# Kernel optimization log

Measured on AMD Instinct MI355X. Metric: run time of the kernel, lower is better.

The kernel has to match this reference:

```python
import jax, jax.numpy as jnp
import numpy as np

HEAD_DIM = 32
KERNEL = 9
DILATION = 3


def setup_inputs() -> dict:
    key = jax.random.key(0)
    k1, k2, k3 = jax.random.split(key, 3)
    B, d, L = 4, 512, 4096
    q = jax.random.normal(k1, (B, d, 1, L), dtype=jnp.float32)
    k = jax.random.normal(k2, (B, d, 1, L), dtype=jnp.float32)
    v = jax.random.normal(k3, (B, d, 1, L), dtype=jnp.float32)
    return {"q": q, "k": k, "v": v}


def reference(q, k, v):
    # q,k,v: [B, d, 1, L]; output: [B, 1, L, d]
    B, d, _, N = q.shape
    hd = HEAD_DIM
    h = d // hd
    K = KERNEL
    dil = DILATION
    pad = dil * (K - 1) // 2
    scale = hd ** -0.5

    # Window gather indices replicating nn.Unfold with zero padding.
    idx = jnp.arange(N)[:, None] + jnp.arange(K)[None, :] * dil - pad  # [N, K]
    valid = ((idx >= 0) & (idx < N)).astype(q.dtype)                   # [N, K]
    idxc = jnp.clip(idx, 0, N - 1)

    qr = q.reshape(B, h, hd, N)
    kr = k.reshape(B, h, hd, N)
    vr = v.reshape(B, h, hd, N)

    # Unfolded windows: [B, h, hd, N, K], zero outside bounds (like Unfold padding)
    kw = kr[:, :, :, idxc] * valid
    vw = vr[:, :, :, idxc] * valid

    attn = jnp.einsum('bhdn,bhdnk->bhnk', qr, kw) * scale
    attn = jax.nn.softmax(attn, axis=-1)
    out = jnp.einsum('bhnk,bhdnk->bhnd', attn, vw)  # [B, h, N, hd]
    # torch: transpose(1,2).reshape(B,1,N,d) -> heads concatenated per token
    return out.transpose(0, 2, 1, 3).reshape(B, 1, N, d)
```

## Files before the change

kernel.cpp:

```cpp
#include <hip/hip_runtime.h>
#include <math.h>

#define NPOS 4096
#define DCH  512
#define HD   32
#define NH   16
#define KW   9
#define DIL  3
#define PAD  12
#define TILE   32
#define NTILES (NPOS / TILE)
#define SPANT  (TILE + 2*PAD)
#define RS     60
#define ROWC   (RS / 4)
#define NCHK   (2 * HD * ROWC)
#define NINST  (NCHK / 64)
#define CSPL   8
#define CPT    (HD / CSPL)
#define TPT    4
#define WSPAN  28
#define NXCD   8

typedef float floatx4 __attribute__((ext_vector_type(4)));

__device__ __forceinline__ void gload16(const float* g, float* l) {
    __builtin_amdgcn_global_load_lds(
        (const __attribute__((address_space(1))) void*)g,
        (__attribute__((address_space(3))) void*)l,
        16, 0, 0);
}

__device__ __forceinline__ float dpp_sum8(float x) {
    int t;
    t = __builtin_amdgcn_update_dpp(0, __float_as_int(x), 0xB1, 0xF, 0xF, true);
    x += __int_as_float(t);
    t = __builtin_amdgcn_update_dpp(0, __float_as_int(x), 0x4E, 0xF, 0xF, true);
    x += __int_as_float(t);
    t = __builtin_amdgcn_update_dpp(0, __float_as_int(x), 0x141, 0xF, 0xF, true);
    x += __int_as_float(t);
    return x;
}

__device__ __forceinline__ void load_w(const float* base, float* w) {
    const float4* wp = (const float4*)base;
#pragma unroll
    for (int u = 0; u < WSPAN / 4; ++u) {
        float4 x = wp[u];
        w[4*u] = x.x; w[4*u+1] = x.y; w[4*u+2] = x.z; w[4*u+3] = x.w;
    }
}

__global__ __launch_bounds__(64) void dilate_attn_kernel(
    const float* __restrict__ q,
    const float* __restrict__ k,
    const float* __restrict__ v,
    float* __restrict__ out)
{
    __shared__ float kv[2 * HD * RS];

    const int id   = blockIdx.x;
    const int xcd  = id & (NXCD - 1);
    const int seq  = id >> 3;
    const int tile = seq & (NTILES - 1);
    const int bh   = ((seq >> 7) << 3) | xcd;

    const int n0t  = tile * TILE;
    const int ws   = n0t - PAD;

    const size_t cb = (size_t)bh * HD * NPOS;
    const float* qg = q + cb;
    const float* kg = k + cb;
    const float* vg = v + cb;

    const int tid = threadIdx.x;
    const int cs  = tid & (CSPL - 1);
    const int lg  = tid >> 3;
    const int n0  = n0t + lg * TPT;

    const float scale = 0.17677669529663687f;

    float4 qv[CPT];
#pragma unroll
    for (int i = 0; i < CPT; ++i)
        qv[i] = *(const float4*)(qg + (size_t)(cs * CPT + i) * NPOS + n0);
    asm volatile("" ::: "memory");

#pragma unroll
    for (int it = 0; it < NINST; ++it) {
        int c   = it * 64 + tid;
        int row = c / ROWC;
        int c4  = c - row * ROWC;
        int g0  = min(max(ws + c4 * 4, 0), NPOS - 4);
        const float* src = (row < HD)
            ? kg + (size_t)row * NPOS + g0
            : vg + (size_t)(row - HD) * NPOS + g0;
        gload16(src, &kv[c * 4]);
    }

    asm volatile("s_waitcnt vmcnt(7)" ::: "memory");

    float s[TPT][KW];
#pragma unroll
    for (int t = 0; t < TPT; ++t)
#pragma unroll
        for (int j = 0; j < KW; ++j) s[t][j] = 0.0f;

#pragma unroll
    for (int i = 0; i < CPT; ++i) {
        int row = cs * CPT + i;
        float w[WSPAN];
        load_w(&kv[row * RS + lg * TPT], w);
        float qt[TPT] = {qv[i].x, qv[i].y, qv[i].z, qv[i].w};
#pragma unroll
        for (int t = 0; t < TPT; ++t)
#pragma unroll
            for (int j = 0; j < KW; ++j)
                s[t][j] = fmaf(qt[t], w[t + 3*j], s[t][j]);
    }

#pragma unroll
    for (int t = 0; t < TPT; ++t)
#pragma unroll
        for (int j = 0; j < KW; ++j)
            s[t][j] = dpp_sum8(s[t][j]);

    const bool masked = (tile == 0) || (tile == NTILES - 1);
    if (!masked) {
#pragma unroll
        for (int t = 0; t < TPT; ++t) {
            float m = -INFINITY;
#pragma unroll
            for (int j = 0; j < KW; ++j) {
                float x = s[t][j] * scale;
                s[t][j] = x;
                m = fmaxf(m, x);
            }
            float sum = 0.0f;
#pragma unroll
            for (int j = 0; j < KW; ++j) {
                float e = __expf(s[t][j] - m);
                s[t][j] = e;
                sum += e;
            }
            float inv = 1.0f / sum;
#pragma unroll
            for (int j = 0; j < KW; ++j) s[t][j] *= inv;
        }
    } else {
#pragma unroll
        for (int t = 0; t < TPT; ++t) {
            float vm[KW];
            float m = -INFINITY;
#pragma unroll
            for (int j = 0; j < KW; ++j) {
                vm[j] = ((unsigned)(n0 + t + 3*j - PAD) < NPOS) ? 1.0f : 0.0f;
                float x = s[t][j] * scale * vm[j];
                s[t][j] = x;
                m = fmaxf(m, x);
            }
            float sum = 0.0f;
#pragma unroll
            for (int j = 0; j < KW; ++j) {
                float e = __expf(s[t][j] - m);
                s[t][j] = e;
                sum += e;
            }
            float inv = 1.0f / sum;
#pragma unroll
            for (int j = 0; j < KW; ++j)
                s[t][j] *= inv * vm[j];
        }
    }

    asm volatile("s_waitcnt vmcnt(0)" ::: "memory");

    float o[TPT][CPT];
#pragma unroll
    for (int t = 0; t < TPT; ++t)
#pragma unroll
        for (int i = 0; i < CPT; ++i) o[t][i] = 0.0f;

#pragma unroll
    for (int i = 0; i < CPT; ++i) {
        int row = cs * CPT + i;
        float w[WSPAN];
        load_w(&kv[(HD + row) * RS + lg * TPT], w);
#pragma unroll
        for (int t = 0; t < TPT; ++t)
#pragma unroll
            for (int j = 0; j < KW; ++j)
                o[t][i] = fmaf(s[t][j], w[t + 3*j], o[t][i]);
    }

    const int b  = bh >> 4;
    const int hh = bh & (NH - 1);
#pragma unroll
    for (int t = 0; t < TPT; ++t) {
        float* op = out + ((size_t)(b * NPOS + n0 + t)) * DCH + hh * HD + cs * CPT;
        floatx4 val = {o[t][0], o[t][1], o[t][2], o[t][3]};
        __builtin_nontemporal_store(val, (floatx4*)op);
    }
}

extern "C" void kernel_launch(void* const* d_in, const int* in_sizes, int n_in,
                              void* d_out, int out_size, void* d_ws, size_t ws_size,
                              hipStream_t stream) {
    const float* q = (const float*)d_in[0];
    const float* k = (const float*)d_in[1];
    const float* v = (const float*)d_in[2];
    float* out = (float*)d_out;

    const int grid = 4 * NH * NTILES;
    hipLaunchKernelGGL(dilate_attn_kernel, dim3(grid), dim3(64), 0, stream,
                       q, k, v, out);
}
```

Before: 132.4 us.

## Load V rows directly into registers with double-buffered prefetch instead of LDS

Only the K window is staged in shared memory now, which halves LDS per block. Each lane reads its V window rows straight from global memory into two register buffers, and the loads are interleaved with the QK and softmax math so V latency overlaps compute. Launch bounds add a minimum of 4 blocks per CU, aiming for higher occupancy. The cost is redundant, overlapping global loads across lanes, served from cache, plus more register pressure from holding two 28-float buffers.

```diff
diff --git a/kernel.cpp b/kernel.cpp
--- a/kernel.cpp
+++ b/kernel.cpp
@@ -13,12 +13,13 @@
 #define SPANT  (TILE + 2*PAD)
 #define RS     60
 #define ROWC   (RS / 4)
-#define NCHK   (2 * HD * ROWC)
-#define NINST  (NCHK / 64)
+#define KCHK   (HD * ROWC)
+#define KINST  8
 #define CSPL   8
 #define CPT    (HD / CSPL)
 #define TPT    4
 #define WSPAN  28
+#define WCHK   (WSPAN / 4)
 #define NXCD   8
 
 typedef float floatx4 __attribute__((ext_vector_type(4)));
@@ -41,22 +42,22 @@
     return x;
 }
 
-__device__ __forceinline__ void load_w(const float* base, float* w) {
-    const float4* wp = (const float4*)base;
-#pragma unroll
-    for (int u = 0; u < WSPAN / 4; ++u) {
-        float4 x = wp[u];
+__device__ __forceinline__ void vload_row(const float* row, int w0, float* w) {
+#pragma unroll
+    for (int u = 0; u < WCHK; ++u) {
+        int g0 = min(max(w0 + 4 * u, 0), NPOS - 4);
+        float4 x = *(const float4*)(row + g0);
         w[4*u] = x.x; w[4*u+1] = x.y; w[4*u+2] = x.z; w[4*u+3] = x.w;
     }
 }
 
-__global__ __launch_bounds__(64) void dilate_attn_kernel(
+__global__ __launch_bounds__(64, 4) void dilate_attn_kernel(
     const float* __restrict__ q,
     const float* __restrict__ k,
     const float* __restrict__ v,
     float* __restrict__ out)
 {
-    __shared__ float kv[2 * HD * RS];
+    __shared__ float ks[HD * RS];
 
     const int id   = blockIdx.x;
     const int xcd  = id & (NXCD - 1);
@@ -76,6 +77,7 @@
     const int cs  = tid & (CSPL - 1);
     const int lg  = tid >> 3;
     const int n0  = n0t + lg * TPT;
+    const int w0  = n0 - PAD;
 
     const float scale = 0.17677669529663687f;
 
@@ -86,16 +88,20 @@
     asm volatile("" ::: "memory");
 
 #pragma unroll
-    for (int it = 0; it < NINST; ++it) {
-        int c   = it * 64 + tid;
-        int row = c / ROWC;
-        int c4  = c - row * ROWC;
-        int g0  = min(max(ws + c4 * 4, 0), NPOS - 4);
-        const float* src = (row < HD)
-            ? kg + (size_t)row * NPOS + g0
-            : vg + (size_t)(row - HD) * NPOS + g0;
-        gload16(src, &kv[c * 4]);
-    }
+    for (int it = 0; it < KINST; ++it) {
+        int c = it * 64 + tid;
+        if (c < KCHK) {
+            int row = c / ROWC;
+            int c4  = c - row * ROWC;
+            int g0  = min(max(ws + c4 * 4, 0), NPOS - 4);
+            gload16(kg + (size_t)row * NPOS + g0, &ks[c * 4]);
+        }
+    }
+    asm volatile("" ::: "memory");
+
+    float vA[WSPAN], vB[WSPAN];
+    vload_row(vg + (size_t)(cs * CPT + 0) * NPOS, w0, vA);
+    asm volatile("" ::: "memory");
 
     asm volatile("s_waitcnt vmcnt(7)" ::: "memory");
 
@@ -109,7 +115,12 @@
     for (int i = 0; i < CPT; ++i) {
         int row = cs * CPT + i;
         float w[WSPAN];
-        load_w(&kv[row * RS + lg * TPT], w);
+        const float4* wp = (const float4*)&ks[row * RS + lg * TPT];
+#pragma unroll
+        for (int u = 0; u < WCHK; ++u) {
+            float4 x = wp[u];
+            w[4*u] = x.x; w[4*u+1] = x.y; w[4*u+2] = x.z; w[4*u+3] = x.w;
+        }
         float qt[TPT] = {qv[i].x, qv[i].y, qv[i].z, qv[i].w};
 #pragma unroll
         for (int t = 0; t < TPT; ++t)
@@ -117,6 +128,8 @@
             for (int j = 0; j < KW; ++j)
                 s[t][j] = fmaf(qt[t], w[t + 3*j], s[t][j]);
     }
+
+    vload_row(vg + (size_t)(cs * CPT + 1) * NPOS, w0, vB);
 
 #pragma unroll
     for (int t = 0; t < TPT; ++t)
@@ -172,8 +185,6 @@
         }
     }
 
-    asm volatile("s_waitcnt vmcnt(0)" ::: "memory");
-
     float o[TPT][CPT];
 #pragma unroll
     for (int t = 0; t < TPT; ++t)
@@ -181,16 +192,30 @@
         for (int i = 0; i < CPT; ++i) o[t][i] = 0.0f;
 
 #pragma unroll
-    for (int i = 0; i < CPT; ++i) {
-        int row = cs * CPT + i;
-        float w[WSPAN];
-        load_w(&kv[(HD + row) * RS + lg * TPT], w);
-#pragma unroll
-        for (int t = 0; t < TPT; ++t)
-#pragma unroll
-            for (int j = 0; j < KW; ++j)
-                o[t][i] = fmaf(s[t][j], w[t + 3*j], o[t][i]);
-    }
+    for (int t = 0; t < TPT; ++t)
+#pragma unroll
+        for (int j = 0; j < KW; ++j)
+            o[t][0] = fmaf(s[t][j], vA[t + 3*j], o[t][0]);
+    vload_row(vg + (size_t)(cs * CPT + 2) * NPOS, w0, vA);
+
+#pragma unroll
+    for (int t = 0; t < TPT; ++t)
+#pragma unroll
+        for (int j = 0; j < KW; ++j)
+            o[t][1] = fmaf(s[t][j], vB[t + 3*j], o[t][1]);
+    vload_row(vg + (size_t)(cs * CPT + 3) * NPOS, w0, vB);
+
+#pragma unroll
+    for (int t = 0; t < TPT; ++t)
+#pragma unroll
+        for (int j = 0; j < KW; ++j)
+            o[t][2] = fmaf(s[t][j], vA[t + 3*j], o[t][2]);
+
+#pragma unroll
+    for (int t = 0; t < TPT; ++t)
+#pragma unroll
+        for (int j = 0; j < KW; ++j)
+            o[t][3] = fmaf(s[t][j], vB[t + 3*j], o[t][3]);
 
     const int b  = bh >> 4;
     const int hh = bh & (NH - 1);
```

New measurement: 221.0 us. 66.9% more time.

## Process four tiles per block with double-buffered LDS prefetch of next tile

Applied to the files above, without the earlier changes.

Each 64-thread block now walks four consecutive sequence tiles of one (batch, head). It keeps two LDS buffers so the K/V window and q values for the next tile are fetched asynchronously while the current tile is computed. Hand-tuned s_waitcnt counts gate each stage. This aims to hide global-load latency inside a block instead of relying on many short-lived blocks. In exchange the grid shrinks fourfold, which cuts available wave-level parallelism, and LDS use doubles.

```diff
diff --git a/kernel.cpp b/kernel.cpp
--- a/kernel.cpp
+++ b/kernel.cpp
@@ -10,6 +10,8 @@
 #define PAD  12
 #define TILE   32
 #define NTILES (NPOS / TILE)
+#define TPB    4
+#define NBLK   (NTILES / TPB)
 #define SPANT  (TILE + 2*PAD)
 #define RS     60
 #define ROWC   (RS / 4)
@@ -19,6 +21,7 @@
 #define CPT    (HD / CSPL)
 #define TPT    4
 #define WSPAN  28
+#define WCHK   (WSPAN / 4)
 #define NXCD   8
 
 typedef float floatx4 __attribute__((ext_vector_type(4)));
@@ -41,50 +44,8 @@
     return x;
 }
 
-__device__ __forceinline__ void load_w(const float* base, float* w) {
-    const float4* wp = (const float4*)base;
-#pragma unroll
-    for (int u = 0; u < WSPAN / 4; ++u) {
-        float4 x = wp[u];
-        w[4*u] = x.x; w[4*u+1] = x.y; w[4*u+2] = x.z; w[4*u+3] = x.w;
-    }
-}
-
-__global__ __launch_bounds__(64) void dilate_attn_kernel(
-    const float* __restrict__ q,
-    const float* __restrict__ k,
-    const float* __restrict__ v,
-    float* __restrict__ out)
-{
-    __shared__ float kv[2 * HD * RS];
-
-    const int id   = blockIdx.x;
-    const int xcd  = id & (NXCD - 1);
-    const int seq  = id >> 3;
-    const int tile = seq & (NTILES - 1);
-    const int bh   = ((seq >> 7) << 3) | xcd;
-
-    const int n0t  = tile * TILE;
-    const int ws   = n0t - PAD;
-
-    const size_t cb = (size_t)bh * HD * NPOS;
-    const float* qg = q + cb;
-    const float* kg = k + cb;
-    const float* vg = v + cb;
-
-    const int tid = threadIdx.x;
-    const int cs  = tid & (CSPL - 1);
-    const int lg  = tid >> 3;
-    const int n0  = n0t + lg * TPT;
-
-    const float scale = 0.17677669529663687f;
-
-    float4 qv[CPT];
-#pragma unroll
-    for (int i = 0; i < CPT; ++i)
-        qv[i] = *(const float4*)(qg + (size_t)(cs * CPT + i) * NPOS + n0);
-    asm volatile("" ::: "memory");
-
+__device__ __forceinline__ void stage_kv(const float* kg, const float* vg,
+                                         int ws, int tid, float* buf) {
 #pragma unroll
     for (int it = 0; it < NINST; ++it) {
         int c   = it * 64 + tid;
@@ -94,111 +55,179 @@
         const float* src = (row < HD)
             ? kg + (size_t)row * NPOS + g0
             : vg + (size_t)(row - HD) * NPOS + g0;
-        gload16(src, &kv[c * 4]);
+        gload16(src, buf + c * 4);
     }
-
-    asm volatile("s_waitcnt vmcnt(7)" ::: "memory");
-
-    float s[TPT][KW];
-#pragma unroll
-    for (int t = 0; t < TPT; ++t)
-#pragma unroll
-        for (int j = 0; j < KW; ++j) s[t][j] = 0.0f;
-
-#pragma unroll
-    for (int i = 0; i < CPT; ++i) {
-        int row = cs * CPT + i;
-        float w[WSPAN];
-        load_w(&kv[row * RS + lg * TPT], w);
-        float qt[TPT] = {qv[i].x, qv[i].y, qv[i].z, qv[i].w};
-#pragma unroll
-        for (int t = 0; t < TPT; ++t)
+}
+
+__global__ __launch_bounds__(64) void dilate_attn_kernel(
+    const float* __restrict__ q,
+    const float* __restrict__ k,
+    const float* __restrict__ v,
+    float* __restrict__ out)
+{
+    __shared__ float kv[2][2 * HD * RS];
+
+    const int id  = blockIdx.x;
+    const int xcd = id & (NXCD - 1);
+    const int seq = id >> 3;
+    const int tg  = seq & (NBLK - 1);
+    const int bh  = ((seq >> 5) << 3) | xcd;
+    const int t0  = tg * TPB;
+
+    const size_t cb = (size_t)bh * HD * NPOS;
+    const float* qg = q + cb;
+    const float* kg = k + cb;
+    const float* vg = v + cb;
+
+    const int tid = threadIdx.x;
+    const int cs  = tid & (CSPL - 1);
+    const int lg  = tid >> 3;
+    const int b   = bh >> 4;
+    const int hh  = bh & (NH - 1);
+
+    const float scale = 0.17677669529663687f;
+
+    float4 qv[2][CPT];
+
+#pragma unroll
+    for (int i = 0; i < CPT; ++i)
+        qv[0][i] = *(const float4*)(qg + (size_t)(cs * CPT + i) * NPOS
+                                    + t0 * TILE + lg * TPT);
+    asm volatile("" ::: "memory");
+    stage_kv(kg, vg, t0 * TILE - PAD, tid, kv[0]);
+    asm volatile("" ::: "memory");
+
+#pragma unroll
+    for (int t = 0; t < TPB; ++t) {
+        const int tile = t0 + t;
+        const int n0   = tile * TILE + lg * TPT;
+        float* buf = kv[t & 1];
+
+        if (t < TPB - 1) {
+#pragma unroll
+            for (int i = 0; i < CPT; ++i)
+                qv[(t + 1) & 1][i] =
+                    *(const float4*)(qg + (size_t)(cs * CPT + i) * NPOS
+                                     + (tile + 1) * TILE + lg * TPT);
+            asm volatile("" ::: "memory");
+            stage_kv(kg, vg, (tile + 1) * TILE - PAD, tid, kv[(t + 1) & 1]);
+            asm volatile("" ::: "memory");
+        }
+
+        if (t == 0)           asm volatile("s_waitcnt vmcnt(19)" ::: "memory");
+        else if (t < TPB - 1) asm volatile("s_waitcnt vmcnt(23)" ::: "memory");
+        else                  asm volatile("s_waitcnt vmcnt(4)"  ::: "memory");
+
+        float s[TPT][KW];
+#pragma unroll
+        for (int tt = 0; tt < TPT; ++tt)
+#pragma unroll
+            for (int j = 0; j < KW; ++j) s[tt][j] = 0.0f;
+
+#pragma unroll
+        for (int i = 0; i < CPT; ++i) {
+            int row = cs * CPT + i;
+            float w[WSPAN];
+            const float4* wp = (const float4*)&buf[row * RS + lg * TPT];
+#pragma unroll
+            for (int u = 0; u < WCHK; ++u) {
+                float4 x = wp[u];
+                w[4*u] = x.x; w[4*u+1] = x.y; w[4*u+2] = x.z; w[4*u+3] = x.w;
+            }
+            float qt[TPT] = {qv[t & 1][i].x, qv[t & 1][i].y,
+                             qv[t & 1][i].z, qv[t & 1][i].w};
+#pragma unroll
+            for (int tt = 0; tt < TPT; ++tt)
+#pragma unroll
+                for (int j = 0; j < KW; ++j)
+                    s[tt][j] = fmaf(qt[tt], w[tt + 3*j], s[tt][j]);
+        }
+
+#pragma unroll
+        for (int tt = 0; tt < TPT; ++tt)
 #pragma unroll
             for (int j = 0; j < KW; ++j)
-                s[t][j] = fmaf(qt[t], w[t + 3*j], s[t][j]);
-    }
-
-#pragma unroll
-    for (int t = 0; t < TPT; ++t)
-#pragma unroll
-        for (int j = 0; j < KW; ++j)
-            s[t][j] = dpp_sum8(s[t][j]);
-
-    const bool masked = (tile == 0) || (tile == NTILES - 1);
-    if (!masked) {
-#pragma unroll
-        for (int t = 0; t < TPT; ++t) {
-            float m = -INFINITY;
-#pragma unroll
-            for (int j = 0; j < KW; ++j) {
-                float x = s[t][j] * scale;
-                s[t][j] = x;
-                m = fmaxf(m, x);
-            }
-            float sum = 0.0f;
-#pragma unroll
-            for (int j = 0; j < KW; ++j) {
-                float e = __expf(s[t][j] - m);
-                s[t][j] = e;
-                sum += e;
-            }
-            float inv = 1.0f / sum;
-#pragma unroll
-            for (int j = 0; j < KW; ++j) s[t][j] *= inv;
-        }
-    } else {
-#pragma unroll
-        for (int t = 0; t < TPT; ++t) {
-            float vm[KW];
-            float m = -INFINITY;
-#pragma unroll
-            for (int j = 0; j < KW; ++j) {
-                vm[j] = ((unsigned)(n0 + t + 3*j - PAD) < NPOS) ? 1.0f : 0.0f;
-                float x = s[t][j] * scale * vm[j];
-                s[t][j] = x;
-                m = fmaxf(m, x);
-            }
-            float sum = 0.0f;
-#pragma unroll
-            for (int j = 0; j < KW; ++j) {
-                float e = __expf(s[t][j] - m);
-                s[t][j] = e;
-                sum += e;
-            }
-            float inv = 1.0f / sum;
-#pragma unroll
-            for (int j = 0; j < KW; ++j)
-                s[t][j] *= inv * vm[j];
-        }
-    }
-
-    asm volatile("s_waitcnt vmcnt(0)" ::: "memory");
-
-    float o[TPT][CPT];
-#pragma unroll
-    for (int t = 0; t < TPT; ++t)
-#pragma unroll
-        for (int i = 0; i < CPT; ++i) o[t][i] = 0.0f;
-
-#pragma unroll
-    for (int i = 0; i < CPT; ++i) {
-        int row = cs * CPT + i;
-        float w[WSPAN];
-        load_w(&kv[(HD + row) * RS + lg * TPT], w);
-#pragma unroll
-        for (int t = 0; t < TPT; ++t)
-#pragma unroll
-            for (int j = 0; j < KW; ++j)
-                o[t][i] = fmaf(s[t][j], w[t + 3*j], o[t][i]);
-    }
-
-    const int b  = bh >> 4;
-    const int hh = bh & (NH - 1);
-#pragma unroll
-    for (int t = 0; t < TPT; ++t) {
-        float* op = out + ((size_t)(b * NPOS + n0 + t)) * DCH + hh * HD + cs * CPT;
-        floatx4 val = {o[t][0], o[t][1], o[t][2], o[t][3]};
-        __builtin_nontemporal_store(val, (floatx4*)op);
+                s[tt][j] = dpp_sum8(s[tt][j]);
+
+        const bool masked = (tile == 0) || (tile == NTILES - 1);
+        if (!masked) {
+#pragma unroll
+            for (int tt = 0; tt < TPT; ++tt) {
+                float m = -INFINITY;
+#pragma unroll
+                for (int j = 0; j < KW; ++j) {
+                    float x = s[tt][j] * scale;
+                    s[tt][j] = x;
+                    m = fmaxf(m, x);
+                }
+                float sum = 0.0f;
+#pragma unroll
+                for (int j = 0; j < KW; ++j) {
+                    float e = __expf(s[tt][j] - m);
+                    s[tt][j] = e;
+                    sum += e;
+                }
+                float inv = 1.0f / sum;
+#pragma unroll
+                for (int j = 0; j < KW; ++j) s[tt][j] *= inv;
+            }
+        } else {
+#pragma unroll
+            for (int tt = 0; tt < TPT; ++tt) {
+                float vm[KW];
+                float m = -INFINITY;
+#pragma unroll
+                for (int j = 0; j < KW; ++j) {
+                    vm[j] = ((unsigned)(n0 + tt + 3*j - PAD) < NPOS) ? 1.0f : 0.0f;
+                    float x = s[tt][j] * scale * vm[j];
+                    s[tt][j] = x;
+                    m = fmaxf(m, x);
+                }
+                float sum = 0.0f;
+#pragma unroll
+                for (int j = 0; j < KW; ++j) {
+                    float e = __expf(s[tt][j] - m);
+                    s[tt][j] = e;
+                    sum += e;
+                }
+                float inv = 1.0f / sum;
+#pragma unroll
+                for (int j = 0; j < KW; ++j)
+                    s[tt][j] *= inv * vm[j];
+            }
+        }
+
+        float o[TPT][CPT];
+#pragma unroll
+        for (int tt = 0; tt < TPT; ++tt)
+#pragma unroll
+            for (int i = 0; i < CPT; ++i) o[tt][i] = 0.0f;
+
+#pragma unroll
+        for (int i = 0; i < CPT; ++i) {
+            int row = cs * CPT + i;
+            float w[WSPAN];
+            const float4* wp = (const float4*)&buf[(HD + row) * RS + lg * TPT];
+#pragma unroll
+            for (int u = 0; u < WCHK; ++u) {
+                float4 x = wp[u];
+                w[4*u] = x.x; w[4*u+1] = x.y; w[4*u+2] = x.z; w[4*u+3] = x.w;
+            }
+#pragma unroll
+            for (int tt = 0; tt < TPT; ++tt)
+#pragma unroll
+                for (int j = 0; j < KW; ++j)
+                    o[tt][i] = fmaf(s[tt][j], w[tt + 3*j], o[tt][i]);
+        }
+
+#pragma unroll
+        for (int tt = 0; tt < TPT; ++tt) {
+            float* op = out + ((size_t)(b * NPOS + n0 + tt)) * DCH
+                        + hh * HD + cs * CPT;
+            floatx4 val = {o[tt][0], o[tt][1], o[tt][2], o[tt][3]};
+            __builtin_nontemporal_store(val, (floatx4*)op);
+        }
+        asm volatile("" ::: "memory");
     }
 }
 
@@ -210,7 +239,7 @@
     const float* v = (const float*)d_in[2];
     float* out = (float*)d_out;
 
-    const int grid = 4 * NH * NTILES;
+    const int grid = 4 * NH * NBLK;
     hipLaunchKernelGGL(dilate_attn_kernel, dim3(grid), dim3(64), 0, stream,
                        q, k, v, out);
 }
```

Result: slower. 145.7 us (+10.0%).
